# Kernel tuning notes

Measured on AMD Instinct MI355X. Metric: run time of the kernel, lower is better.

The kernel has to match this reference:

```python
import jax, jax.numpy as jnp
import numpy as np

N = 50000      # nodes
E = 500000     # edges
D_IN = 512
D_H = 512
D_OUT = 256


def setup_inputs() -> dict:
    key = jax.random.key(0)
    ks = jax.random.split(key, 5)
    x = jax.random.normal(ks[0], (N, D_IN), dtype=jnp.float32)
    edge_index = jax.random.randint(ks[1], (2, E), 0, N, dtype=jnp.int32)
    W1 = jax.random.normal(ks[2], (D_IN, D_H), dtype=jnp.float32) / np.float32(np.sqrt(D_IN))
    b1 = jnp.zeros((D_H,), dtype=jnp.float32)
    W2 = jax.random.normal(ks[3], (D_H, D_OUT), dtype=jnp.float32) / np.float32(np.sqrt(D_H))
    b2 = jnp.zeros((D_OUT,), dtype=jnp.float32)
    return {"x": x, "edge_index": edge_index, "W1": W1, "b1": b1, "W2": W2, "b2": b2}


def _gcn_conv(x, src, dst, W, b, n):
    # PyG GCNConv: h = X W; add self-loops; symmetric norm D^-1/2 (A+I) D^-1/2; aggregate at dst; + bias
    h = x @ W
    loop = jnp.arange(n, dtype=src.dtype)
    src_sl = jnp.concatenate([src, loop])
    dst_sl = jnp.concatenate([dst, loop])
    deg = jax.ops.segment_sum(jnp.ones_like(src_sl, dtype=h.dtype), dst_sl, num_segments=n)
    dinv = jnp.where(deg > 0, jax.lax.rsqrt(deg), 0.0)
    norm = dinv[src_sl] * dinv[dst_sl]                     # [E+N]
    msg = h[src_sl] * norm[:, None]                        # [E+N, out]
    out = jax.ops.segment_sum(msg, dst_sl, num_segments=n) # [N, out]
    return out + b


def reference(x, edge_index, W1, b1, W2, b2):
    # Encoder.forward in eval mode (dropout = identity, bn='none' = identity), ELU activation after each conv.
    src, dst = edge_index[0], edge_index[1]
    h = _gcn_conv(x, src, dst, W1, b1, N)
    h = jax.nn.elu(h)
    h = _gcn_conv(h, src, dst, W2, b2, N)
    return jax.nn.elu(h)
```

## Files before the change

kernel.cpp:

```cpp
#include <hip/hip_runtime.h>
#include <math.h>

#define N_NODES 50000
#define N_EDGES 500000
#define D_IN 512
#define D_H  512
#define D_OUT 256
#define NB 196

typedef __attribute__((ext_vector_type(8))) short bf16x8;
typedef __attribute__((ext_vector_type(8))) unsigned short ushort8;
typedef __attribute__((ext_vector_type(4))) float f32x4;

__device__ __forceinline__ float b2f(unsigned short u) {
    union { unsigned int i; float f; } v; v.i = ((unsigned int)u) << 16; return v.f;
}
__device__ __forceinline__ unsigned short f2b(float f) {
    unsigned int x = __float_as_uint(f);
    unsigned int r = (x + 0x7fffu + ((x >> 16) & 1u)) >> 16;
    return (unsigned short)r;
}


__global__ void k_wt(const float* __restrict__ W, unsigned short* __restrict__ Wt,
                     int K, int N) {
    __shared__ float t[32][33];
    const int bk = blockIdx.x * 32, bn = blockIdx.y * 32;
    const int tx = threadIdx.x, ty = threadIdx.y;
    for (int i = ty; i < 32; i += 8) t[i][tx] = W[(size_t)(bk + i) * N + bn + tx];
    __syncthreads();
    for (int i = ty; i < 32; i += 8)
        Wt[(size_t)(bn + i) * K + bk + tx] = f2b(t[tx][i]);
}


__global__ __launch_bounds__(256) void k_zero(int* __restrict__ p, int n) {
    int i = blockIdx.x * 256 + threadIdx.x;
    if (i < n) p[i] = 0;
}

__global__ __launch_bounds__(256) void k_indeg(const int* __restrict__ dst,
                                               int* __restrict__ indeg) {
    int i = blockIdx.x * 256 + threadIdx.x;
    if (i < N_EDGES) atomicAdd(&indeg[dst[i]], 1);
}

__global__ __launch_bounds__(256) void k_partials(const int* __restrict__ indeg,
                                                  int* __restrict__ bsum) {
    __shared__ int wsum[4];
    const int tid = threadIdx.x, lane = tid & 63, w = tid >> 6;
    const int i = blockIdx.x * 256 + tid;
    int v = (i < N_NODES) ? indeg[i] : 0;
#pragma unroll
    for (int o = 32; o > 0; o >>= 1) v += __shfl_down(v, o, 64);
    if (lane == 0) wsum[w] = v;
    __syncthreads();
    if (tid == 0) bsum[blockIdx.x] = wsum[0] + wsum[1] + wsum[2] + wsum[3];
}

__global__ __launch_bounds__(256) void k_scanb(const int* __restrict__ bsum,
                                               int* __restrict__ boff) {
    __shared__ int wsum[4];
    const int tid = threadIdx.x, lane = tid & 63, w = tid >> 6;
    const int v = (tid < NB) ? bsum[tid] : 0;
    int s = v;
#pragma unroll
    for (int o = 1; o < 64; o <<= 1) {
        int t = __shfl_up(s, o, 64);
        if (lane >= o) s += t;
    }
    if (lane == 63) wsum[w] = s;
    __syncthreads();
    int add = 0;
    for (int k = 0; k < w; ++k) add += wsum[k];
    if (tid < NB) boff[tid] = add + s - v;
}

__global__ __launch_bounds__(256) void k_finalize(const int* __restrict__ indeg,
                                                  const int* __restrict__ boff,
                                                  int* __restrict__ row_start,
                                                  int* __restrict__ cursor,
                                                  float* __restrict__ dinv) {
    __shared__ int wsum[4];
    const int tid = threadIdx.x, lane = tid & 63, w = tid >> 6;
    const int i = blockIdx.x * 256 + tid;
    const int v = (i < N_NODES) ? indeg[i] : 0;
    int s = v;
#pragma unroll
    for (int o = 1; o < 64; o <<= 1) {
        int t = __shfl_up(s, o, 64);
        if (lane >= o) s += t;
    }
    if (lane == 63) wsum[w] = s;
    __syncthreads();
    int add = boff[blockIdx.x];
    for (int k = 0; k < w; ++k) add += wsum[k];
    if (i < N_NODES) {
        const int excl = add + s - v;
        row_start[i] = excl;
        cursor[i] = excl;
        dinv[i] = rsqrtf((float)(1 + v));
    }
    if (i == N_NODES) row_start[N_NODES] = N_EDGES;
}

__global__ __launch_bounds__(256) void k_bucket(const int* __restrict__ src,
                                                const int* __restrict__ dst,
                                                int* __restrict__ cursor,
                                                int* __restrict__ csr_src) {
    int e = blockIdx.x * 256 + threadIdx.x;
    if (e >= N_EDGES) return;
    int pos = atomicAdd(&cursor[dst[e]], 1);
    csr_src[pos] = src[e];
}


__device__ __forceinline__ void gload16(const void* g, void* l) {
    __builtin_amdgcn_global_load_lds(
        (const __attribute__((address_space(1))) unsigned int*)g,
        (__attribute__((address_space(3))) unsigned int*)l, 16, 0, 0);
}

template <bool A32>
__global__ __launch_bounds__(512, 2) void k_gemm256(const void* __restrict__ Av,
                                                    const unsigned short* __restrict__ Bt,
                                                    unsigned short* __restrict__ C,
                                                    int M, int N, int K) {
    __shared__ __align__(16) short As[2][256 * 32];
    __shared__ __align__(16) short Bs[2][256 * 32];

    const int tid = threadIdx.x;
    const int wid = tid >> 6;
    const int lane = tid & 63;
    const int wr = wid >> 2;
    const int wc = wid & 3;
    const int brow = blockIdx.y * 256;
    const int bcol = blockIdx.x * 256;
    const int lhi = lane >> 4;
    const int llo = lane & 15;
    const int sw = (lhi ^ (llo & 3)) * 8;

    f32x4 acc[8][4];
#pragma unroll
    for (int i = 0; i < 8; ++i)
#pragma unroll
        for (int j = 0; j < 4; ++j) acc[i][j] = (f32x4){0.f, 0.f, 0.f, 0.f};

    const float* Af = (const float*)Av;
    const unsigned short* Ab = (const unsigned short*)Av;

    const int arow = tid >> 1;
    const int ach0 = (tid & 1) * 2;
    int gra = brow + arow;
    gra = gra < M ? gra : M - 1;
    const float* aptr32 = Af + (size_t)gra * K;
    const int awch0 = (ach0 ^ (arow & 3)) * 8;
    const int awch1 = ((ach0 + 1) ^ (arow & 3)) * 8;

    const int nt = K / 32;

#define STAGE_B(buf, kt)                                                          \
    {                                                                             \
        _Pragma("unroll")                                                         \
        for (int g = 0; g < 2; ++g) {                                             \
            const int cbase = g * 512 + wid * 64;                                 \
            const int c = cbase + lane;                                           \
            const int row = c >> 2;                                               \
            const int sc = (c & 3) ^ (row & 3);                                   \
            gload16(Bt + (size_t)(bcol + row) * K + (kt) * 32 + sc * 8,           \
                    &Bs[buf][cbase * 8]);                                         \
        }                                                                         \
    }
#define STAGE_A_BF16(buf, kt)                                                     \
    {                                                                             \
        _Pragma("unroll")                                                         \
        for (int g = 0; g < 2; ++g) {                                             \
            const int cbase = g * 512 + wid * 64;                                 \
            const int c = cbase + lane;                                           \
            int row = c >> 2;                                                     \
            const int sc = (c & 3) ^ (row & 3);                                   \
            int gr = brow + row;                                                  \
            gr = gr < M ? gr : M - 1;                                             \
            gload16(Ab + (size_t)gr * K + (kt) * 32 + sc * 8,                     \
                    &As[buf][cbase * 8]);                                         \
        }                                                                         \
    }

    if (A32) {
        const float4 a0 = *(const float4*)(aptr32 + ach0 * 8);
        const float4 a1 = *(const float4*)(aptr32 + ach0 * 8 + 4);
        const float4 a2 = *(const float4*)(aptr32 + ach0 * 8 + 8);
        const float4 a3 = *(const float4*)(aptr32 + ach0 * 8 + 12);
        STAGE_B(0, 0);
        ushort8 u0, u1;
        u0[0] = f2b(a0.x); u0[1] = f2b(a0.y); u0[2] = f2b(a0.z); u0[3] = f2b(a0.w);
        u0[4] = f2b(a1.x); u0[5] = f2b(a1.y); u0[6] = f2b(a1.z); u0[7] = f2b(a1.w);
        u1[0] = f2b(a2.x); u1[1] = f2b(a2.y); u1[2] = f2b(a2.z); u1[3] = f2b(a2.w);
        u1[4] = f2b(a3.x); u1[5] = f2b(a3.y); u1[6] = f2b(a3.z); u1[7] = f2b(a3.w);
        *(ushort8*)&As[0][arow * 32 + awch0] = u0;
        *(ushort8*)&As[0][arow * 32 + awch1] = u1;
    } else {
        STAGE_A_BF16(0, 0);
        STAGE_B(0, 0);
    }
    __syncthreads();

    int cur = 0;
    for (int t = 0; t < nt; ++t) {
        const bool more = (t + 1 < nt);
        float4 a0, a1, a2, a3;
        if (more) {
            const int ktn = (t + 1) * 32;
            if (A32) {
                a0 = *(const float4*)(aptr32 + ktn + ach0 * 8);
                a1 = *(const float4*)(aptr32 + ktn + ach0 * 8 + 4);
                a2 = *(const float4*)(aptr32 + ktn + ach0 * 8 + 8);
                a3 = *(const float4*)(aptr32 + ktn + ach0 * 8 + 12);
            } else {
                STAGE_A_BF16(cur ^ 1, t + 1);
            }
            STAGE_B(cur ^ 1, t + 1);
        }

        bf16x8 af[8], bf[4];
#pragma unroll
        for (int mi = 0; mi < 8; ++mi)
            af[mi] = *(const bf16x8*)&As[cur][(wr * 128 + mi * 16 + llo) * 32 + sw];
#pragma unroll
        for (int ni = 0; ni < 4; ++ni)
            bf[ni] = *(const bf16x8*)&Bs[cur][(wc * 64 + ni * 16 + llo) * 32 + sw];
#pragma unroll
        for (int mi = 0; mi < 8; ++mi)
#pragma unroll
            for (int ni = 0; ni < 4; ++ni)
                acc[mi][ni] = __builtin_amdgcn_mfma_f32_16x16x32_bf16(
                    af[mi], bf[ni], acc[mi][ni], 0, 0, 0);

        if (A32 && more) {
            ushort8 u0, u1;
            u0[0] = f2b(a0.x); u0[1] = f2b(a0.y); u0[2] = f2b(a0.z); u0[3] = f2b(a0.w);
            u0[4] = f2b(a1.x); u0[5] = f2b(a1.y); u0[6] = f2b(a1.z); u0[7] = f2b(a1.w);
            u1[0] = f2b(a2.x); u1[1] = f2b(a2.y); u1[2] = f2b(a2.z); u1[3] = f2b(a2.w);
            u1[4] = f2b(a3.x); u1[5] = f2b(a3.y); u1[6] = f2b(a3.z); u1[7] = f2b(a3.w);
            *(ushort8*)&As[cur ^ 1][arow * 32 + awch0] = u0;
            *(ushort8*)&As[cur ^ 1][arow * 32 + awch1] = u1;
        }

        __syncthreads();
        cur ^= 1;
    }

#pragma unroll
    for (int mi = 0; mi < 8; ++mi) {
        const int row0 = brow + wr * 128 + mi * 16 + lhi * 4;
#pragma unroll
        for (int ni = 0; ni < 4; ++ni) {
            const int col = bcol + wc * 64 + ni * 16 + llo;
            const f32x4 v = acc[mi][ni];
#pragma unroll
            for (int r = 0; r < 4; ++r) {
                const int row = row0 + r;
                if (row < M) C[(size_t)row * N + col] = f2b(v[r]);
            }
        }
    }
#undef STAGE_B
#undef STAGE_A_BF16
}


template <int D, bool BF16_OUT>
__global__ __launch_bounds__(256) void k_aggregate(const unsigned short* __restrict__ H,
                                                   const float* __restrict__ bias,
                                                   void* __restrict__ outv,
                                                   const int* __restrict__ row_start,
                                                   const int* __restrict__ csr_src,
                                                   const float* __restrict__ dinv) {
    const int wid = threadIdx.x >> 6;
    const int lane = threadIdx.x & 63;
    int n, c0;
    if (D == 512) { n = blockIdx.x * 4 + wid; c0 = lane * 8; }
    else          { n = blockIdx.x * 8 + wid * 2 + (lane >> 5); c0 = (lane & 31) * 8; }
    if (n >= N_NODES) return;

    const float di = dinv[n];
    float acc[8];
    {
        const float ws = di * di;
        ushort8 v = *(const ushort8*)(H + (size_t)n * D + c0);
#pragma unroll
        for (int e = 0; e < 8; ++e) acc[e] = b2f(v[e]) * ws;
    }

    const int e0 = row_start[n];
    const int e1 = row_start[n + 1];
    int j = e0;
    for (; j + 8 <= e1; j += 8) {
        int s[8];
        float wgt[8];
#pragma unroll
        for (int q = 0; q < 8; ++q) s[q] = csr_src[j + q];
#pragma unroll
        for (int q = 0; q < 8; ++q) wgt[q] = dinv[s[q]] * di;
#pragma unroll
        for (int h = 0; h < 2; ++h) {
            const ushort8 v0 = *(const ushort8*)(H + (size_t)s[h * 4 + 0] * D + c0);
            const ushort8 v1 = *(const ushort8*)(H + (size_t)s[h * 4 + 1] * D + c0);
            const ushort8 v2 = *(const ushort8*)(H + (size_t)s[h * 4 + 2] * D + c0);
            const ushort8 v3 = *(const ushort8*)(H + (size_t)s[h * 4 + 3] * D + c0);
#pragma unroll
            for (int e = 0; e < 8; ++e) {
                acc[e] = fmaf(b2f(v0[e]), wgt[h * 4 + 0], acc[e]);
                acc[e] = fmaf(b2f(v1[e]), wgt[h * 4 + 1], acc[e]);
                acc[e] = fmaf(b2f(v2[e]), wgt[h * 4 + 2], acc[e]);
                acc[e] = fmaf(b2f(v3[e]), wgt[h * 4 + 3], acc[e]);
            }
        }
    }
    for (; j + 4 <= e1; j += 4) {
        const int s0 = csr_src[j + 0];
        const int s1 = csr_src[j + 1];
        const int s2 = csr_src[j + 2];
        const int s3 = csr_src[j + 3];
        const float w0 = dinv[s0] * di;
        const float w1 = dinv[s1] * di;
        const float w2 = dinv[s2] * di;
        const float w3 = dinv[s3] * di;
        const ushort8 v0 = *(const ushort8*)(H + (size_t)s0 * D + c0);
        const ushort8 v1 = *(const ushort8*)(H + (size_t)s1 * D + c0);
        const ushort8 v2 = *(const ushort8*)(H + (size_t)s2 * D + c0);
        const ushort8 v3 = *(const ushort8*)(H + (size_t)s3 * D + c0);
#pragma unroll
        for (int e = 0; e < 8; ++e) {
            acc[e] = fmaf(b2f(v0[e]), w0, acc[e]);
            acc[e] = fmaf(b2f(v1[e]), w1, acc[e]);
            acc[e] = fmaf(b2f(v2[e]), w2, acc[e]);
            acc[e] = fmaf(b2f(v3[e]), w3, acc[e]);
        }
    }
    for (; j < e1; ++j) {
        const int s = csr_src[j];
        const float ws = dinv[s] * di;
        const ushort8 v = *(const ushort8*)(H + (size_t)s * D + c0);
#pragma unroll
        for (int e = 0; e < 8; ++e) acc[e] = fmaf(b2f(v[e]), ws, acc[e]);
    }

#pragma unroll
    for (int e = 0; e < 8; ++e) {
        float t = acc[e] + bias[c0 + e];
        acc[e] = t > 0.f ? t : expf(t) - 1.f;
    }

    if (BF16_OUT) {
        ushort8 o;
#pragma unroll
        for (int e = 0; e < 8; ++e) o[e] = f2b(acc[e]);
        *(ushort8*)((unsigned short*)outv + (size_t)n * D + c0) = o;
    } else {
        float* orow = (float*)outv + (size_t)n * D + c0;
        *(float4*)orow = make_float4(acc[0], acc[1], acc[2], acc[3]);
        *(float4*)(orow + 4) = make_float4(acc[4], acc[5], acc[6], acc[7]);
    }
}


extern "C" void kernel_launch(void* const* d_in, const int* in_sizes, int n_in,
                              void* d_out, int out_size, void* d_ws, size_t ws_size,
                              hipStream_t stream) {
    const float* x  = (const float*)d_in[0];
    const int* ei   = (const int*)d_in[1];
    const int* src  = ei;
    const int* dst  = ei + N_EDGES;
    const float* W1 = (const float*)d_in[2];
    const float* b1 = (const float*)d_in[3];
    const float* W2 = (const float*)d_in[4];
    const float* b2 = (const float*)d_in[5];
    float* out = (float*)d_out;

    char* ws = (char*)d_ws;
    size_t off = 0;
    auto alloc = [&](size_t bytes) -> void* {
        void* p = ws + off;
        off = (off + bytes + 255) & ~(size_t)255;
        return p;
    };
    int*   indeg     = (int*)alloc((size_t)N_NODES * 4);
    int*   bsum      = (int*)alloc((size_t)NB * 4);
    int*   boff      = (int*)alloc((size_t)NB * 4);
    int*   row_start = (int*)alloc((size_t)(N_NODES + 1) * 4);
    int*   cursor    = (int*)alloc((size_t)N_NODES * 4);
    int*   csr_src   = (int*)alloc((size_t)N_EDGES * 4);
    float* dinv      = (float*)alloc((size_t)N_NODES * 4);
    unsigned short* W1t  = (unsigned short*)alloc((size_t)D_H * D_IN * 2);
    unsigned short* W2t  = (unsigned short*)alloc((size_t)D_OUT * D_H * 2);
    unsigned short* H1   = (unsigned short*)alloc((size_t)N_NODES * D_H * 2);
    unsigned short* out1 = (unsigned short*)alloc((size_t)N_NODES * D_H * 2);
    unsigned short* H2   = (unsigned short*)alloc((size_t)N_NODES * D_OUT * 2);

    k_zero<<<(N_NODES + 255) / 256, 256, 0, stream>>>(indeg, N_NODES);
    k_indeg<<<(N_EDGES + 255) / 256, 256, 0, stream>>>(dst, indeg);
    k_partials<<<NB, 256, 0, stream>>>(indeg, bsum);
    k_scanb<<<1, 256, 0, stream>>>(bsum, boff);
    k_finalize<<<NB, 256, 0, stream>>>(indeg, boff, row_start, cursor, dinv);
    k_bucket<<<(N_EDGES + 255) / 256, 256, 0, stream>>>(src, dst, cursor, csr_src);

    {
        dim3 b(32, 8);
        dim3 g1(D_IN / 32, D_H / 32);
        k_wt<<<g1, b, 0, stream>>>(W1, W1t, D_IN, D_H);
        dim3 g2(D_H / 32, D_OUT / 32);
        k_wt<<<g2, b, 0, stream>>>(W2, W2t, D_H, D_OUT);
    }

    const int nmb = (N_NODES + 255) / 256;

    {
        dim3 g(D_H / 256, nmb);
        k_gemm256<true><<<g, 512, 0, stream>>>(x, W1t, H1, N_NODES, D_H, D_IN);
    }
    k_aggregate<512, true><<<(N_NODES + 3) / 4, 256, 0, stream>>>(H1, b1, out1, row_start, csr_src, dinv);

    {
        dim3 g(D_OUT / 256, nmb);
        k_gemm256<false><<<g, 512, 0, stream>>>(out1, W2t, H2, N_NODES, D_OUT, D_H);
    }
    k_aggregate<256, false><<<(N_NODES + 7) / 8, 256, 0, stream>>>(H2, b2, out, row_start, csr_src, dinv);
}
```

Baseline: 314.9 us.

## Switch GEMM to 128x128 tiles with K=64 stages and 256 threads

Replaces the 256x256-tile, 512-thread GEMM with a 128x128-tile, 256-thread kernel. Each stage now covers 64 of K instead of 32, with an XOR swizzle over 8 chunks in LDS. The fp32 A operand is loaded through registers in a reshaped per-thread pattern before bf16 conversion. The goal is more blocks (better CU fill on the 50000-row problem) and fewer sync points per K, at the cost of less operand reuse per tile.

```diff
diff --git a/kernel.cpp b/kernel.cpp
--- a/kernel.cpp
+++ b/kernel.cpp
@@ -122,85 +122,85 @@
 }
 
 template <bool A32>
-__global__ __launch_bounds__(512, 2) void k_gemm256(const void* __restrict__ Av,
-                                                    const unsigned short* __restrict__ Bt,
-                                                    unsigned short* __restrict__ C,
-                                                    int M, int N, int K) {
-    __shared__ __align__(16) short As[2][256 * 32];
-    __shared__ __align__(16) short Bs[2][256 * 32];
+__global__ __launch_bounds__(256, 2) void k_gemm(const void* __restrict__ Av,
+                                                 const unsigned short* __restrict__ Bt,
+                                                 unsigned short* __restrict__ C,
+                                                 int M, int N, int K) {
+    __shared__ __align__(16) short As[2][128 * 64];
+    __shared__ __align__(16) short Bs[2][128 * 64];
 
     const int tid = threadIdx.x;
     const int wid = tid >> 6;
     const int lane = tid & 63;
-    const int wr = wid >> 2;
-    const int wc = wid & 3;
-    const int brow = blockIdx.y * 256;
-    const int bcol = blockIdx.x * 256;
-    const int lhi = lane >> 4;
-    const int llo = lane & 15;
-    const int sw = (lhi ^ (llo & 3)) * 8;
-
-    f32x4 acc[8][4];
-#pragma unroll
-    for (int i = 0; i < 8; ++i)
+    const int wr = wid >> 1, wc = wid & 1;
+    const int brow = blockIdx.y * 128;
+    const int bcol = blockIdx.x * 128;
+    const int lhi = lane >> 4, llo = lane & 15;
+
+    f32x4 acc[4][4];
+#pragma unroll
+    for (int i = 0; i < 4; ++i)
 #pragma unroll
         for (int j = 0; j < 4; ++j) acc[i][j] = (f32x4){0.f, 0.f, 0.f, 0.f};
 
     const float* Af = (const float*)Av;
     const unsigned short* Ab = (const unsigned short*)Av;
 
-    const int arow = tid >> 1;
-    const int ach0 = (tid & 1) * 2;
-    int gra = brow + arow;
-    gra = gra < M ? gra : M - 1;
-    const float* aptr32 = Af + (size_t)gra * K;
-    const int awch0 = (ach0 ^ (arow & 3)) * 8;
-    const int awch1 = ((ach0 + 1) ^ (arow & 3)) * 8;
-
-    const int nt = K / 32;
-
-#define STAGE_B(buf, kt)                                                          \
-    {                                                                             \
-        _Pragma("unroll")                                                         \
-        for (int g = 0; g < 2; ++g) {                                             \
-            const int cbase = g * 512 + wid * 64;                                 \
-            const int c = cbase + lane;                                           \
-            const int row = c >> 2;                                               \
-            const int sc = (c & 3) ^ (row & 3);                                   \
-            gload16(Bt + (size_t)(bcol + row) * K + (kt) * 32 + sc * 8,           \
-                    &Bs[buf][cbase * 8]);                                         \
-        }                                                                         \
-    }
-#define STAGE_A_BF16(buf, kt)                                                     \
-    {                                                                             \
-        _Pragma("unroll")                                                         \
-        for (int g = 0; g < 2; ++g) {                                             \
-            const int cbase = g * 512 + wid * 64;                                 \
-            const int c = cbase + lane;                                           \
-            int row = c >> 2;                                                     \
-            const int sc = (c & 3) ^ (row & 3);                                   \
-            int gr = brow + row;                                                  \
-            gr = gr < M ? gr : M - 1;                                             \
-            gload16(Ab + (size_t)gr * K + (kt) * 32 + sc * 8,                     \
-                    &As[buf][cbase * 8]);                                         \
-        }                                                                         \
-    }
+    float4 ar[4][2];
+
+#define STAGE_B(buf, kt)                                                        \
+    {                                                                           \
+        _Pragma("unroll") for (int g = 0; g < 4; ++g) {                         \
+            const int s = g * 256 + tid;                                        \
+            const int row = s >> 3;                                             \
+            const int sc = (s & 7) ^ (row & 7);                                 \
+            gload16(Bt + (size_t)(bcol + row) * K + (kt) + sc * 8,              \
+                    &Bs[buf][(g * 256 + wid * 64) * 8]);                        \
+        }                                                                       \
+    }
+#define STAGE_A16(buf, kt)                                                      \
+    {                                                                           \
+        _Pragma("unroll") for (int g = 0; g < 4; ++g) {                         \
+            const int s = g * 256 + tid;                                        \
+            const int row = s >> 3;                                             \
+            const int sc = (s & 7) ^ (row & 7);                                 \
+            int gr = brow + row; gr = gr < M ? gr : M - 1;                      \
+            gload16(Ab + (size_t)gr * K + (kt) + sc * 8,                        \
+                    &As[buf][(g * 256 + wid * 64) * 8]);                        \
+        }                                                                       \
+    }
+#define LOAD_A32(kt)                                                            \
+    {                                                                           \
+        _Pragma("unroll") for (int g = 0; g < 4; ++g) {                         \
+            const int s = g * 256 + tid;                                        \
+            const int row = s >> 3;                                             \
+            const int sc = (s & 7) ^ (row & 7);                                 \
+            int gr = brow + row; gr = gr < M ? gr : M - 1;                      \
+            const float* p = Af + (size_t)gr * K + (kt) + sc * 8;               \
+            ar[g][0] = *(const float4*)p;                                       \
+            ar[g][1] = *(const float4*)(p + 4);                                 \
+        }                                                                       \
+    }
+#define WRITE_A32(buf)                                                          \
+    {                                                                           \
+        _Pragma("unroll") for (int g = 0; g < 4; ++g) {                         \
+            ushort8 u;                                                          \
+            u[0] = f2b(ar[g][0].x); u[1] = f2b(ar[g][0].y);                     \
+            u[2] = f2b(ar[g][0].z); u[3] = f2b(ar[g][0].w);                     \
+            u[4] = f2b(ar[g][1].x); u[5] = f2b(ar[g][1].y);                     \
+            u[6] = f2b(ar[g][1].z); u[7] = f2b(ar[g][1].w);                     \
+            *(ushort8*)&As[buf][(g * 256 + tid) * 8] = u;                       \
+        }                                                                       \
+    }
+
+    const int nt = K / 64;
 
     if (A32) {
-        const float4 a0 = *(const float4*)(aptr32 + ach0 * 8);
-        const float4 a1 = *(const float4*)(aptr32 + ach0 * 8 + 4);
-        const float4 a2 = *(const float4*)(aptr32 + ach0 * 8 + 8);
-        const float4 a3 = *(const float4*)(aptr32 + ach0 * 8 + 12);
+        LOAD_A32(0);
         STAGE_B(0, 0);
-        ushort8 u0, u1;
-        u0[0] = f2b(a0.x); u0[1] = f2b(a0.y); u0[2] = f2b(a0.z); u0[3] = f2b(a0.w);
-        u0[4] = f2b(a1.x); u0[5] = f2b(a1.y); u0[6] = f2b(a1.z); u0[7] = f2b(a1.w);
-        u1[0] = f2b(a2.x); u1[1] = f2b(a2.y); u1[2] = f2b(a2.z); u1[3] = f2b(a2.w);
-        u1[4] = f2b(a3.x); u1[5] = f2b(a3.y); u1[6] = f2b(a3.z); u1[7] = f2b(a3.w);
-        *(ushort8*)&As[0][arow * 32 + awch0] = u0;
-        *(ushort8*)&As[0][arow * 32 + awch1] = u1;
+        WRITE_A32(0);
     } else {
-        STAGE_A_BF16(0, 0);
+        STAGE_A16(0, 0);
         STAGE_B(0, 0);
     }
     __syncthreads();
@@ -208,51 +208,45 @@
     int cur = 0;
     for (int t = 0; t < nt; ++t) {
         const bool more = (t + 1 < nt);
-        float4 a0, a1, a2, a3;
         if (more) {
-            const int ktn = (t + 1) * 32;
             if (A32) {
-                a0 = *(const float4*)(aptr32 + ktn + ach0 * 8);
-                a1 = *(const float4*)(aptr32 + ktn + ach0 * 8 + 4);
-                a2 = *(const float4*)(aptr32 + ktn + ach0 * 8 + 8);
-                a3 = *(const float4*)(aptr32 + ktn + ach0 * 8 + 12);
+                LOAD_A32((t + 1) * 64);
             } else {
-                STAGE_A_BF16(cur ^ 1, t + 1);
+                STAGE_A16(cur ^ 1, (t + 1) * 64);
             }
-            STAGE_B(cur ^ 1, t + 1);
+            STAGE_B(cur ^ 1, (t + 1) * 64);
         }
 
-        bf16x8 af[8], bf[4];
-#pragma unroll
-        for (int mi = 0; mi < 8; ++mi)
-            af[mi] = *(const bf16x8*)&As[cur][(wr * 128 + mi * 16 + llo) * 32 + sw];
-#pragma unroll
-        for (int ni = 0; ni < 4; ++ni)
-            bf[ni] = *(const bf16x8*)&Bs[cur][(wc * 64 + ni * 16 + llo) * 32 + sw];
-#pragma unroll
-        for (int mi = 0; mi < 8; ++mi)
-#pragma unroll
-            for (int ni = 0; ni < 4; ++ni)
-                acc[mi][ni] = __builtin_amdgcn_mfma_f32_16x16x32_bf16(
-                    af[mi], bf[ni], acc[mi][ni], 0, 0, 0);
-
-        if (A32 && more) {
-            ushort8 u0, u1;
-            u0[0] = f2b(a0.x); u0[1] = f2b(a0.y); u0[2] = f2b(a0.z); u0[3] = f2b(a0.w);
-            u0[4] = f2b(a1.x); u0[5] = f2b(a1.y); u0[6] = f2b(a1.z); u0[7] = f2b(a1.w);
-            u1[0] = f2b(a2.x); u1[1] = f2b(a2.y); u1[2] = f2b(a2.z); u1[3] = f2b(a2.w);
-            u1[4] = f2b(a3.x); u1[5] = f2b(a3.y); u1[6] = f2b(a3.z); u1[7] = f2b(a3.w);
-            *(ushort8*)&As[cur ^ 1][arow * 32 + awch0] = u0;
-            *(ushort8*)&As[cur ^ 1][arow * 32 + awch1] = u1;
+#pragma unroll
+        for (int ks = 0; ks < 2; ++ks) {
+            bf16x8 af[4], bf[4];
+#pragma unroll
+            for (int mi = 0; mi < 4; ++mi) {
+                const int row = wr * 64 + mi * 16 + llo;
+                af[mi] = *(const bf16x8*)&As[cur][row * 64 + (((ks * 4 + lhi) ^ (llo & 7)) * 8)];
+            }
+#pragma unroll
+            for (int ni = 0; ni < 4; ++ni) {
+                const int row = wc * 64 + ni * 16 + llo;
+                bf[ni] = *(const bf16x8*)&Bs[cur][row * 64 + (((ks * 4 + lhi) ^ (llo & 7)) * 8)];
+            }
+#pragma unroll
+            for (int mi = 0; mi < 4; ++mi)
+#pragma unroll
+                for (int ni = 0; ni < 4; ++ni)
+                    acc[mi][ni] = __builtin_amdgcn_mfma_f32_16x16x32_bf16(
+                        af[mi], bf[ni], acc[mi][ni], 0, 0, 0);
         }
+
+        if (A32 && more) WRITE_A32(cur ^ 1);
 
         __syncthreads();
         cur ^= 1;
     }
 
 #pragma unroll
-    for (int mi = 0; mi < 8; ++mi) {
-        const int row0 = brow + wr * 128 + mi * 16 + lhi * 4;
+    for (int mi = 0; mi < 4; ++mi) {
+        const int row0 = brow + wr * 64 + mi * 16 + lhi * 4;
 #pragma unroll
         for (int ni = 0; ni < 4; ++ni) {
             const int col = bcol + wc * 64 + ni * 16 + llo;
@@ -265,7 +259,9 @@
         }
     }
 #undef STAGE_B
-#undef STAGE_A_BF16
+#undef STAGE_A16
+#undef LOAD_A32
+#undef WRITE_A32
 }
 
 
@@ -413,17 +409,17 @@
         k_wt<<<g2, b, 0, stream>>>(W2, W2t, D_H, D_OUT);
     }
 
-    const int nmb = (N_NODES + 255) / 256;
+    const int nrb = (N_NODES + 127) / 128;
 
     {
-        dim3 g(D_H / 256, nmb);
-        k_gemm256<true><<<g, 512, 0, stream>>>(x, W1t, H1, N_NODES, D_H, D_IN);
+        dim3 g(D_H / 128, nrb);
+        k_gemm<true><<<g, 256, 0, stream>>>(x, W1t, H1, N_NODES, D_H, D_IN);
     }
     k_aggregate<512, true><<<(N_NODES + 3) / 4, 256, 0, stream>>>(H1, b1, out1, row_start, csr_src, dinv);
 
     {
-        dim3 g(D_OUT / 256, nmb);
-        k_gemm256<false><<<g, 512, 0, stream>>>(out1, W2t, H2, N_NODES, D_OUT, D_H);
+        dim3 g(D_OUT / 128, nrb);
+        k_gemm<false><<<g, 256, 0, stream>>>(out1, W2t, H2, N_NODES, D_OUT, D_H);
     }
     k_aggregate<256, false><<<(N_NODES + 7) / 8, 256, 0, stream>>>(H2, b2, out, row_start, csr_src, dinv);
 }
```

Measured after the change: 315.2 us. Within noise of the previous version (+0.1%).
